# Performance work log

Hardware: AMD Instinct MI355X
Metric: run time of the kernel (lower is better)

## Reference

```python
import jax, jax.numpy as jnp
import numpy as np

EMBED = 512
HEADS = 8
HEAD_DIM = EMBED // HEADS
SCALE_BASE = 512
NEG = -1e9


def xpos_apply(x, offset, downscale):
    # x: [(b h), L, d]
    L, d = x.shape[1], x.shape[2]
    min_pos = -(L + offset) // 2
    max_pos = L + offset + min_pos
    base = (jnp.arange(0, d, 2, dtype=jnp.float32) + 0.4 * d) / (1.4 * d)      # [d/2]
    power = jnp.arange(min_pos, max_pos, dtype=jnp.float32) / SCALE_BASE        # [L']
    scale = base[None, :] ** power[:, None]                                     # [L', d/2]
    half = d // 2
    inv_freq = 1.0 / (10000.0 ** (jnp.arange(half, dtype=jnp.float32) / half))
    sinusoid = jnp.arange(scale.shape[0], dtype=jnp.float32)[:, None] * inv_freq[None, :]
    sin, cos = jnp.sin(sinusoid), jnp.cos(sinusoid)
    # keep last L rows (no-op when offset == 0)
    scale, sin, cos = scale[-L:], sin[-L:], cos[-L:]
    if downscale:
        scale = 1.0 / scale
    sin2 = jnp.repeat(sin * scale, 2, axis=-1)   # duplicate_interleave -> [L, d]
    cos2 = jnp.repeat(cos * scale, 2, axis=-1)
    x1, x2 = x[..., ::2], x[..., 1::2]
    rot = jnp.stack([-x2, x1], axis=-1).reshape(x.shape)  # rotate_every_two
    return x * cos2[None] + rot * sin2[None]


def split_heads(x, b, L):
    # 'b l (h d) -> (b h) l d'
    return x.reshape(b, L, HEADS, HEAD_DIM).transpose(0, 2, 1, 3).reshape(b * HEADS, L, HEAD_DIM)


def setup_inputs() -> dict:
    key = jax.random.key(0)
    ks = jax.random.split(key, 12)
    b, L = 4, 2048
    inp = {
        'query': jax.random.normal(ks[0], (b, L, EMBED), jnp.float32),
        'key': jax.random.normal(ks[1], (b, L, EMBED), jnp.float32),
        'value': jax.random.normal(ks[2], (b, L, EMBED), jnp.float32),
        'key_padding_mask': jnp.zeros((b, L), jnp.bool_),
        'attn_mask': jnp.where(jnp.tril(jnp.ones((L, L), jnp.bool_)), 0.0, NEG).astype(jnp.float32),
    }
    s = 1.0 / np.sqrt(EMBED)
    inp['Wq'] = jax.random.normal(ks[3], (EMBED, EMBED), jnp.float32) * s
    inp['bq'] = jnp.zeros((EMBED,), jnp.float32)
    inp['Wk'] = jax.random.normal(ks[4], (EMBED, EMBED), jnp.float32) * s
    inp['bk'] = jnp.zeros((EMBED,), jnp.float32)
    inp['Wv'] = jax.random.normal(ks[5], (EMBED, EMBED), jnp.float32) * s
    inp['bv'] = jnp.zeros((EMBED,), jnp.float32)
    inp['Wo'] = jax.random.normal(ks[6], (EMBED, EMBED), jnp.float32) * s
    inp['bo'] = jnp.zeros((EMBED,), jnp.float32)
    return inp


def reference(query, key, value, key_padding_mask, attn_mask, Wq, bq, Wk, bk, Wv, bv, Wo, bo):
    b, L, _ = query.shape
    q = split_heads(query @ Wq.T + bq, b, L)
    k = split_heads(key @ Wk.T + bk, b, L)
    v = split_heads(value @ Wv.T + bv, b, L)
    k = xpos_apply(k, 0, True)
    q = xpos_apply(q, 0, False)
    q = q * (HEAD_DIM ** -0.5)
    aw = jnp.einsum('btd,bsd->bts', q, k)                 # [(b h), t, s]
    aw = jnp.nan_to_num(aw) + attn_mask[None]
    aw = aw.reshape(b, HEADS, L, L)
    aw = jnp.where(key_padding_mask[:, None, None, :], jnp.finfo(aw.dtype).min, aw)
    aw = aw.reshape(b * HEADS, L, L)
    probs = jax.nn.softmax(aw.astype(jnp.float32), axis=-1).astype(aw.dtype)
    attn = jnp.einsum('bts,bsd->btd', probs, v)           # [(b h), t, d]
    attn = attn.reshape(b, HEADS, L, HEAD_DIM).transpose(0, 2, 1, 3).reshape(b, L, EMBED)
    return attn @ Wo.T + bo
```

## Files before the change

### kernel.cpp

```cpp
#include <hip/hip_runtime.h>
#include <hip/hip_bf16.h>

typedef __bf16 bf16x2 __attribute__((ext_vector_type(2)));
typedef __bf16 bf16x4 __attribute__((ext_vector_type(4)));
typedef __bf16 bf16x8 __attribute__((ext_vector_type(8)));
typedef float  f32x4  __attribute__((ext_vector_type(4)));

#define SEQ    2048
#define EMB    512
#define NHEAD  8
#define HD     64
#define NBATCH 4
#define MROWS  (NBATCH*SEQ)
#define QSCALE 0.18033688011112042f
#define INV2PI 0.15915494309189535f
#define TWOPI  6.28318530717958648f
#define NEGFREQ (-0.41524101186092028f)

__device__ __forceinline__ f32x4 mfma16(bf16x8 a, bf16x8 b, f32x4 c) {
  return __builtin_amdgcn_mfma_f32_16x16x32_bf16(a, b, c, 0, 0, 0);
}

typedef __attribute__((address_space(1))) const void gv_t;
typedef __attribute__((address_space(3))) void lv_t;
__device__ __forceinline__ void async16(const void* g, void* l) {
  __builtin_amdgcn_global_load_lds((gv_t*)g, (lv_t*)l, 16, 0, 0);
}

__global__ __launch_bounds__(256) void conv_kernel(const float* __restrict__ q,
                                                   const float* __restrict__ k,
                                                   const float* __restrict__ v,
                                                   const float* __restrict__ wq,
                                                   const float* __restrict__ wk,
                                                   const float* __restrict__ wv,
                                                   const float* __restrict__ wo,
                                                   __bf16* __restrict__ Qf,
                                                   __bf16* __restrict__ Kf,
                                                   __bf16* __restrict__ Vf,
                                                   __bf16* __restrict__ Wb) {
  const int z = blockIdx.y;
  const float* src;
  __bf16* dst;
  size_t i8;
  if (z < 3) {
    src = (z == 0) ? q : (z == 1) ? k : v;
    dst = (z == 0) ? Qf : (z == 1) ? Kf : Vf;
    i8 = ((size_t)blockIdx.x * 256 + threadIdx.x) * 8;
  } else {
    if (blockIdx.x >= 512) return;
    const int zw = blockIdx.x >> 7;
    src = (zw == 0) ? wq : (zw == 1) ? wk : (zw == 2) ? wv : wo;
    dst = Wb + (size_t)zw * (EMB * EMB);
    i8 = ((size_t)(blockIdx.x & 127) * 256 + threadIdx.x) * 8;
  }
  const float4 fa = ((const float4*)(src + i8))[0];
  const float4 fb = ((const float4*)(src + i8))[1];
  bf16x8 h = { (__bf16)fa.x, (__bf16)fa.y, (__bf16)fa.z, (__bf16)fa.w,
               (__bf16)fb.x, (__bf16)fb.y, (__bf16)fb.z, (__bf16)fb.w };
  *(bf16x8*)(dst + i8) = h;
}

__device__ __forceinline__ void gemm_main(const __bf16* __restrict__ A,
                                          const __bf16* __restrict__ W,
                                          __bf16* As, __bf16* Bs,
                                          f32x4 (&acc)[4][4], int m0, int n0) {
  const int tid = threadIdx.x;
  const int wid = tid >> 6, lane = tid & 63;
  const int quad = lane >> 4, l16 = lane & 15;
  const int l7 = l16 & 7;
  const int srow = lane >> 3;
  const int sxor = ((lane & 7) ^ srow) * 8;
  const int wm = (wid >> 1) * 64, wn = (wid & 1) * 64;

  #pragma unroll
  for (int i = 0; i < 4; ++i)
    #pragma unroll
    for (int j = 0; j < 4; ++j) acc[i][j] = (f32x4)(0.0f);

  for (int k0 = 0; k0 < 512; k0 += 64) {
    __syncthreads();
    #pragma unroll
    for (int ii = 0; ii < 4; ++ii) {
      const int r8 = wid * 32 + ii * 8;
      async16(A + (size_t)(m0 + r8 + srow) * 512 + k0 + sxor, &As[r8 * 64]);
      async16(W + (size_t)(n0 + r8 + srow) * 512 + k0 + sxor, &Bs[r8 * 64]);
    }
    __syncthreads();
    #pragma unroll
    for (int ks = 0; ks < 2; ++ks) {
      bf16x8 af[4], bfr[4];
      #pragma unroll
      for (int i = 0; i < 4; ++i)
        af[i] = *(const bf16x8*)&As[(wm + i * 16 + l16) * 64 +
                                    (((quad + ks * 4) ^ l7) * 8)];
      #pragma unroll
      for (int j = 0; j < 4; ++j)
        bfr[j] = *(const bf16x8*)&Bs[(wn + j * 16 + l16) * 64 +
                                     (((quad + ks * 4) ^ l7) * 8)];
      #pragma unroll
      for (int i = 0; i < 4; ++i)
        #pragma unroll
        for (int j = 0; j < 4; ++j)
          acc[i][j] = mfma16(af[i], bfr[j], acc[i][j]);
    }
  }
}

__global__ __launch_bounds__(256) void gemm_proj_kernel(
    const __bf16* __restrict__ Qf, const __bf16* __restrict__ Kf, const __bf16* __restrict__ Vf,
    const __bf16* __restrict__ Wb,
    const float* __restrict__ bq, const float* __restrict__ bk, const float* __restrict__ bv,
    __bf16* __restrict__ Qx, __bf16* __restrict__ Kx, __bf16* __restrict__ Vt) {
  __shared__ __align__(16) char smem[34816];
  __bf16* As = (__bf16*)smem;
  __bf16* Bs = (__bf16*)(smem + 16384);
  __bf16* T  = (__bf16*)smem;

  const int z = blockIdx.z;
  const __bf16* A = (z == 0) ? Qf : (z == 1) ? Kf : Vf;
  const __bf16* W = Wb + (size_t)z * (EMB * EMB);
  const float* bias = (z == 0) ? bq : (z == 1) ? bk : bv;
  const int m0 = blockIdx.y * 128, n0 = blockIdx.x * 128;

  f32x4 acc[4][4];
  gemm_main(A, W, As, Bs, acc, m0, n0);

  const int tid = threadIdx.x;
  const int wid = tid >> 6, lane = tid & 63;
  const int quad = lane >> 4, l16 = lane & 15;
  const int wm = (wid >> 1) * 64, wn = (wid & 1) * 64;

  __syncthreads();

  if (z == 2) {
    #pragma unroll
    for (int j = 0; j < 4; ++j) {
      const float bval = bias[n0 + wn + j * 16 + l16];
      #pragma unroll
      for (int i = 0; i < 4; ++i) {
        bf16x4 p = { (__bf16)(acc[i][j][0] + bval), (__bf16)(acc[i][j][1] + bval),
                     (__bf16)(acc[i][j][2] + bval), (__bf16)(acc[i][j][3] + bval) };
        *(bf16x4*)&T[(wn + j * 16 + l16) * 136 + wm + i * 16 + quad * 4] = p;
      }
    }
    __syncthreads();
    const int nrow = tid >> 1, mh = (tid & 1) << 6;
    bf16x8 vv[8];
    #pragma unroll
    for (int u = 0; u < 8; ++u) vv[u] = *(const bf16x8*)&T[nrow * 136 + mh + u * 8];
    const int n = n0 + nrow, h = n >> 6, d = n & 63;
    const int bb = m0 >> 11, lb2 = (m0 & 2047) + mh;
    __bf16* dst = Vt + ((size_t)(bb * 8 + h) * 64 + d) * 2048 + lb2;
    #pragma unroll
    for (int u = 0; u < 8; ++u) *(bf16x8*)(dst + u * 8) = vv[u];
  } else {
    #pragma unroll
    for (int j = 0; j < 4; ++j) {
      const float bval = bias[n0 + wn + j * 16 + l16];
      #pragma unroll
      for (int i = 0; i < 4; ++i)
        #pragma unroll
        for (int r = 0; r < 4; ++r)
          T[(wm + i * 16 + quad * 4 + r) * 136 + wn + j * 16 + l16] =
              (__bf16)(acc[i][j][r] + bval);
    }
    __syncthreads();
    const int lrow = tid >> 1, half = tid & 1;
    const int gm = m0 + lrow, l = gm & 2047, bb = gm >> 11;
    const int h = (n0 >> 6) + half;
    bf16x8 vv[8];
    #pragma unroll
    for (int u = 0; u < 8; ++u)
      vv[u] = *(const bf16x8*)&T[lrow * 136 + half * 64 + u * 8];
    bf16x8 ov[8];
    const float lf = (float)l;
    const float pw = (lf - 1024.0f) * (1.0f / 512.0f);
    const float qs = (z == 0) ? QSCALE : 1.0f;
    #pragma unroll
    for (int i = 0; i < 32; ++i) {
      const float x1 = (float)vv[i >> 2][(2 * i) & 7];
      const float x2 = (float)vv[i >> 2][(2 * i + 1) & 7];
      const float lb = __log2f((2.0f * i + 25.6f) * (1.0f / 89.6f));
      const float e  = (z == 0) ? (pw * lb) : (-pw * lb);
      const float sc = __builtin_amdgcn_exp2f(e) * qs;
      const float ang = lf * __builtin_amdgcn_exp2f((float)i * NEGFREQ);
      float rev = ang * INV2PI;
      rev -= floorf(rev);
      const float ar = rev * TWOPI;
      const float sn = __sinf(ar) * sc;
      const float cs = __cosf(ar) * sc;
      ov[i >> 2][(2 * i) & 7]     = (__bf16)(x1 * cs - x2 * sn);
      ov[i >> 2][(2 * i + 1) & 7] = (__bf16)(x2 * cs + x1 * sn);
    }
    __bf16* dst = ((z == 0) ? Qx : Kx) + ((size_t)(bb * 8 + h) * 2048 + l) * 64;
    #pragma unroll
    for (int u = 0; u < 8; ++u) *(bf16x8*)(dst + u * 8) = ov[u];
  }
}

__global__ __launch_bounds__(256) void gemm_out_kernel(
    const __bf16* __restrict__ A, const __bf16* __restrict__ W,
    const float* __restrict__ bias, float* __restrict__ C) {
  __shared__ __align__(16) char smem[34816];
  __bf16* As = (__bf16*)smem;
  __bf16* Bs = (__bf16*)(smem + 16384);
  const int m0 = blockIdx.y * 128, n0 = blockIdx.x * 128;
  f32x4 acc[4][4];
  gemm_main(A, W, As, Bs, acc, m0, n0);
  const int tid = threadIdx.x;
  const int wid = tid >> 6, lane = tid & 63;
  const int quad = lane >> 4, l16 = lane & 15;
  const int wm = (wid >> 1) * 64, wn = (wid & 1) * 64;
  #pragma unroll
  for (int j = 0; j < 4; ++j) {
    const int n = n0 + wn + j * 16 + l16;
    const float bval = bias[n];
    #pragma unroll
    for (int i = 0; i < 4; ++i)
      #pragma unroll
      for (int r = 0; r < 4; ++r)
        C[(size_t)(m0 + wm + i * 16 + quad * 4 + r) * 512 + n] = acc[i][j][r] + bval;
  }
}

__global__ __launch_bounds__(256) void flash_kernel(const __bf16* __restrict__ Qx,
                                                    const __bf16* __restrict__ Kx,
                                                    const __bf16* __restrict__ Vt,
                                                    const unsigned char* __restrict__ kpm,
                                                    __bf16* __restrict__ Oa,
                                                    float* __restrict__ PartO,
                                                    float* __restrict__ Pml) {
  __shared__ __align__(16) __bf16 Ks[2][64 * HD];
  __shared__ __align__(16) __bf16 Vs[2][64 * HD];
  __shared__ __align__(16) __bf16 Qs[64 * HD];

  const int tid = threadIdx.x;
  const int wid = tid >> 6;
  const int lane = tid & 63;
  const int quad = lane >> 4;
  const int l16 = lane & 15;
  const int l7 = l16 & 7;
  const int srow = lane >> 3;
  const int sxor = ((lane & 7) ^ srow) * 8;
  const int bh = blockIdx.x;
  const int b = bh >> 3;
  const int y = blockIdx.y;

  int qb, it0, it1, split;
  if (y < 32) {
    qb = 31 - (y >> 1);
    split = 1;
    const int nt = qb + 1, hh = nt >> 1;
    if ((y & 1) == 0) { it0 = 0;  it1 = hh; }
    else              { it0 = hh; it1 = nt; }
  } else {
    qb = 47 - y;
    split = 0;
    it0 = 0; it1 = qb + 1;
  }
  const int q0 = qb * 64;

  const __bf16* Qbase = Qx + (size_t)bh * (SEQ * HD);
  const __bf16* Kbase = Kx + (size_t)bh * (SEQ * HD);
  const __bf16* Vbase = Vt + (size_t)bh * (HD * SEQ);
  __bf16* Pw = Qs + wid * 1024;

  #pragma unroll
  for (int ii = 0; ii < 2; ++ii) {
    const int r0 = wid * 16 + ii * 8;
    async16(Qbase + (size_t)(q0 + r0 + srow) * HD + sxor, &Qs[r0 * HD]);
    async16(Kbase + (size_t)(it0 * 64 + r0 + srow) * HD + sxor, &Ks[0][r0 * HD]);
    async16(Vbase + (size_t)(r0 + srow) * SEQ + it0 * 64 + sxor, &Vs[0][r0 * HD]);
  }
  __syncthreads();
  const bf16x8 qf0 = *(const bf16x8*)&Qs[(wid * 16 + l16) * HD + ((quad ^ l7) * 8)];
  const bf16x8 qf1 = *(const bf16x8*)&Qs[(wid * 16 + l16) * HD + (((quad + 4) ^ l7) * 8)];

  f32x4 o[4];
  #pragma unroll
  for (int i = 0; i < 4; ++i) o[i] = (f32x4)(0.0f);
  float m_run = -1e30f, l_run = 0.0f;
  const int myq = q0 + wid * 16 + l16;

  for (int it = it0; it < it1; ++it) {
    const int kv0 = it << 6;
    const int cur = (it - it0) & 1;
    const __bf16* Kc = &Ks[cur][0];
    const __bf16* Vc = &Vs[cur][0];

    if (it + 1 < it1) {
      const int kn = kv0 + 64;
      #pragma unroll
      for (int ii = 0; ii < 2; ++ii) {
        const int r0 = wid * 16 + ii * 8;
        async16(Kbase + (size_t)(kn + r0 + srow) * HD + sxor, &Ks[cur ^ 1][r0 * HD]);
        async16(Vbase + (size_t)(r0 + srow) * SEQ + kn + sxor, &Vs[cur ^ 1][r0 * HD]);
      }
    }
    const unsigned mine =
        *(const unsigned*)(kpm + b * SEQ + kv0 + ((lane & 15) << 2));

    f32x4 s[4];
    #pragma unroll
    for (int nb = 0; nb < 4; ++nb) s[nb] = (f32x4)(0.0f);
    __builtin_amdgcn_s_setprio(1);
    #pragma unroll
    for (int nb = 0; nb < 4; ++nb) {
      const bf16x8 kf = *(const bf16x8*)&Kc[(nb * 16 + l16) * HD + ((quad ^ l7) * 8)];
      s[nb] = mfma16(kf, qf0, s[nb]);
    }
    #pragma unroll
    for (int nb = 0; nb < 4; ++nb) {
      const bf16x8 kf = *(const bf16x8*)&Kc[(nb * 16 + l16) * HD + (((quad + 4) ^ l7) * 8)];
      s[nb] = mfma16(kf, qf1, s[nb]);
    }
    __builtin_amdgcn_s_setprio(0);

    if (kv0 + 63 > q0 + wid * 16) {
      #pragma unroll
      for (int nb = 0; nb < 4; ++nb)
        #pragma unroll
        for (int r = 0; r < 4; ++r)
          if (kv0 + nb * 16 + quad * 4 + r > myq) s[nb][r] = -1e30f;
    }
    if (__any(mine != 0)) {
      const unsigned char* kp0 = kpm + b * SEQ + kv0;
      #pragma unroll
      for (int nb = 0; nb < 4; ++nb) {
        const unsigned pk = *(const unsigned*)(kp0 + nb * 16 + quad * 4);
        if (pk) {
          if (pk & 0x000000FFu) s[nb][0] = -1e30f;
          if (pk & 0x0000FF00u) s[nb][1] = -1e30f;
          if (pk & 0x00FF0000u) s[nb][2] = -1e30f;
          if (pk & 0xFF000000u) s[nb][3] = -1e30f;
        }
      }
    }

    float mx;
    {
      f32x4 u0, u1;
      #pragma unroll
      for (int r = 0; r < 4; ++r) u0[r] = fmaxf(s[0][r], s[1][r]);
      #pragma unroll
      for (int r = 0; r < 4; ++r) u1[r] = fmaxf(s[2][r], s[3][r]);
      #pragma unroll
      for (int r = 0; r < 4; ++r) u0[r] = fmaxf(u0[r], u1[r]);
      mx = fmaxf(fmaxf(u0[0], u0[1]), fmaxf(u0[2], u0[3]));
    }
    if (__any(mx > m_run)) {
      float rm = fmaxf(mx, __shfl_xor(mx, 16));
      rm = fmaxf(rm, __shfl_xor(rm, 32));
      const float m_new = fmaxf(m_run, rm);
      const float alpha = __builtin_amdgcn_exp2f(m_run - m_new);
      #pragma unroll
      for (int i = 0; i < 4; ++i) o[i] *= alpha;
      l_run *= alpha;
      m_run = m_new;
    }
    #pragma unroll
    for (int nb = 0; nb < 4; ++nb)
      #pragma unroll
      for (int r = 0; r < 4; ++r)
        s[nb][r] = __builtin_amdgcn_exp2f(s[nb][r] - m_run);
    {
      f32x4 v01 = s[0] + s[1];
      f32x4 v23 = s[2] + s[3];
      f32x4 vt = v01 + v23;
      l_run += (vt[0] + vt[1]) + (vt[2] + vt[3]);
    }

    #pragma unroll
    for (int nb = 0; nb < 4; ++nb) {
      bf16x4 p4 = { (__bf16)s[nb][0], (__bf16)s[nb][1],
                    (__bf16)s[nb][2], (__bf16)s[nb][3] };
      *(bf16x4*)&Pw[l16 * 64 + (((nb * 2 + (quad >> 1)) ^ l7) << 3) + (quad & 1) * 4] = p4;
    }

    __builtin_amdgcn_s_setprio(1);
    #pragma unroll
    for (int ks = 0; ks < 2; ++ks) {
      const bf16x8 pf = *(const bf16x8*)&Pw[l16 * 64 + (((ks * 4 + quad) ^ l7) << 3)];
      const int bx = ((quad + ks * 4) ^ l7) * 8;
      #pragma unroll
      for (int j = 0; j < 4; ++j)
        o[j] = mfma16(*(const bf16x8*)&Vc[(j * 16 + l16) * HD + bx], pf, o[j]);
    }
    __builtin_amdgcn_s_setprio(0);

    if (it + 1 < it1) __syncthreads();
  }

  float lt = l_run + __shfl_xor(l_run, 16);
  lt += __shfl_xor(lt, 32);

  if (split) {
    const int tile = (bh * 16 + (qb - 16)) * 2 + (y & 1);
    float* po = PartO + (size_t)tile * 4096;
    #pragma unroll
    for (int i = 0; i < 4; ++i)
      #pragma unroll
      for (int r = 0; r < 4; ++r)
        po[(i * 16 + quad * 4 + r) * 64 + wid * 16 + l16] = o[i][r];
    if (quad == 0) {
      Pml[(size_t)tile * 128 + wid * 16 + l16] = m_run;
      Pml[(size_t)tile * 128 + 64 + wid * 16 + l16] = lt;
    }
    return;
  }

  const float inv_l = 1.0f / lt;
  {
    bf16x4 t0 = { (__bf16)(o[0][0] * inv_l), (__bf16)(o[0][1] * inv_l),
                  (__bf16)(o[0][2] * inv_l), (__bf16)(o[0][3] * inv_l) };
    bf16x4 t1 = { (__bf16)(o[1][0] * inv_l), (__bf16)(o[1][1] * inv_l),
                  (__bf16)(o[1][2] * inv_l), (__bf16)(o[1][3] * inv_l) };
    bf16x4 t2 = { (__bf16)(o[2][0] * inv_l), (__bf16)(o[2][1] * inv_l),
                  (__bf16)(o[2][2] * inv_l), (__bf16)(o[2][3] * inv_l) };
    bf16x4 t3 = { (__bf16)(o[3][0] * inv_l), (__bf16)(o[3][1] * inv_l),
                  (__bf16)(o[3][2] * inv_l), (__bf16)(o[3][3] * inv_l) };
    *(bf16x4*)&Pw[l16 * 64 + (((0 + (quad >> 1)) ^ l7) << 3) + (quad & 1) * 4] = t0;
    *(bf16x4*)&Pw[l16 * 64 + (((2 + (quad >> 1)) ^ l7) << 3) + (quad & 1) * 4] = t1;
    *(bf16x4*)&Pw[l16 * 64 + (((4 + (quad >> 1)) ^ l7) << 3) + (quad & 1) * 4] = t2;
    *(bf16x4*)&Pw[l16 * 64 + (((6 + (quad >> 1)) ^ l7) << 3) + (quad & 1) * 4] = t3;
  }
  const int h = bh & 7;
  #pragma unroll
  for (int ii = 0; ii < 2; ++ii) {
    const int qr = ii * 8 + (lane >> 3);
    const bf16x8 ovv = *(const bf16x8*)&Pw[qr * 64 + (((lane & 7) ^ (qr & 7)) << 3)];
    *(bf16x8*)(Oa + (((size_t)b * SEQ + q0 + wid * 16 + qr) * NHEAD + h) * HD +
               (lane & 7) * 8) = ovv;
  }
}

__global__ __launch_bounds__(256) void combine_kernel(const float* __restrict__ PartO,
                                                      const float* __restrict__ Pml,
                                                      __bf16* __restrict__ Oa) {
  __shared__ __align__(16) __bf16 T[64 * 72];
  const int pair = blockIdx.x;
  const int bh = pair >> 4, qb = 16 + (pair & 15);
  const int b = bh >> 3, h = bh & 7, q0 = qb * 64;
  const float* P0 = PartO + (size_t)pair * 2 * 4096;
  const float* P1 = P0 + 4096;
  const float* ml = Pml + (size_t)pair * 2 * 128;
  const int t = threadIdx.x;
  const int d = t >> 2, qg = (t & 3) * 16;

  float w0[16], w1[16];
  #pragma unroll
  for (int k = 0; k < 16; ++k) {
    const float m0 = ml[qg + k],       l0 = ml[64 + qg + k];
    const float m1 = ml[128 + qg + k], l1 = ml[192 + qg + k];
    const float m = fmaxf(m0, m1);
    const float a0 = __builtin_amdgcn_exp2f(m0 - m);
    const float a1 = __builtin_amdgcn_exp2f(m1 - m);
    const float inv = 1.0f / (a0 * l0 + a1 * l1);
    w0[k] = a0 * inv;
    w1[k] = a1 * inv;
  }
  #pragma unroll
  for (int k = 0; k < 16; ++k) {
    const float v = P0[d * 64 + qg + k] * w0[k] + P1[d * 64 + qg + k] * w1[k];
    T[(qg + k) * 72 + d] = (__bf16)v;
  }
  __syncthreads();
  const int q = t >> 2, dg = (t & 3) * 16;
  const bf16x8 va = *(const bf16x8*)&T[q * 72 + dg];
  const bf16x8 vb = *(const bf16x8*)&T[q * 72 + dg + 8];
  __bf16* dst = Oa + (((size_t)b * SEQ + q0 + q) * NHEAD + h) * HD + dg;
  *(bf16x8*)dst = va;
  *(bf16x8*)(dst + 8) = vb;
}

extern "C" void kernel_launch(void* const* d_in, const int* in_sizes, int n_in,
                              void* d_out, int out_size, void* d_ws, size_t ws_size,
                              hipStream_t stream) {
  (void)in_sizes; (void)n_in; (void)out_size; (void)ws_size;
  const float* query = (const float*)d_in[0];
  const float* key   = (const float*)d_in[1];
  const float* value = (const float*)d_in[2];
  const unsigned char* kpm = (const unsigned char*)d_in[3];
  const float* Wq = (const float*)d_in[5];
  const float* bq = (const float*)d_in[6];
  const float* Wk = (const float*)d_in[7];
  const float* bk = (const float*)d_in[8];
  const float* Wv = (const float*)d_in[9];
  const float* bv = (const float*)d_in[10];
  const float* Wo = (const float*)d_in[11];
  const float* bo = (const float*)d_in[12];
  float* out = (float*)d_out;

  char* ws = (char*)d_ws;
  const size_t SZ = (size_t)MROWS * EMB * 2;
  __bf16* Qf = (__bf16*)(ws);
  __bf16* Kf = (__bf16*)(ws + SZ);
  __bf16* Vf = (__bf16*)(ws + 2 * SZ);
  __bf16* Qx = (__bf16*)(ws + 3 * SZ);
  __bf16* Kx = (__bf16*)(ws + 4 * SZ);
  __bf16* Vt = (__bf16*)(ws + 5 * SZ);
  __bf16* Wb = (__bf16*)(ws + 6 * SZ);
  __bf16* Oa = Qf;
  float* PartO = (float*)(ws + SZ);
  float* Pml = out;

  conv_kernel<<<dim3(2048, 4), dim3(256), 0, stream>>>(
      query, key, value, Wq, Wk, Wv, Wo, Qf, Kf, Vf, Wb);
  gemm_proj_kernel<<<dim3(4, 64, 3), dim3(256), 0, stream>>>(
      Qf, Kf, Vf, Wb, bq, bk, bv, Qx, Kx, Vt);
  flash_kernel<<<dim3(32, 48), dim3(256), 0, stream>>>(
      Qx, Kx, Vt, kpm, Oa, PartO, Pml);
  combine_kernel<<<dim3(512), dim3(256), 0, stream>>>(PartO, Pml, Oa);
  gemm_out_kernel<<<dim3(4, 64), dim3(256), 0, stream>>>(
      Oa, Wb + (size_t)3 * EMB * EMB, bo, out);
}
```

Measured before the change: 221.9 us.

## Load K/V fragments directly from global memory and drop split-KV combine kernel

The flash kernel stops staging K and V tiles in double-buffered shared memory with async copies and block barriers. Each wave now loads its MFMA operand fragments straight from global memory into registers, which relies on L2/L1 for the reuse across the four waves. The split-KV scheme for the long query blocks and the separate combine kernel are removed, so each block walks its full causal range, and launch bounds request four blocks per CU. This removes barriers, LDS traffic and one kernel launch plus the partial-result round trip. In exchange the long-row blocks see worse load balance, and repeated global loads may be latency-bound.

```diff
diff --git a/kernel.cpp b/kernel.cpp
--- a/kernel.cpp
+++ b/kernel.cpp
@@ -223,16 +223,12 @@
   }
 }
 
-__global__ __launch_bounds__(256) void flash_kernel(const __bf16* __restrict__ Qx,
-                                                    const __bf16* __restrict__ Kx,
-                                                    const __bf16* __restrict__ Vt,
-                                                    const unsigned char* __restrict__ kpm,
-                                                    __bf16* __restrict__ Oa,
-                                                    float* __restrict__ PartO,
-                                                    float* __restrict__ Pml) {
-  __shared__ __align__(16) __bf16 Ks[2][64 * HD];
-  __shared__ __align__(16) __bf16 Vs[2][64 * HD];
-  __shared__ __align__(16) __bf16 Qs[64 * HD];
+__global__ __launch_bounds__(256, 4) void flash_kernel(const __bf16* __restrict__ Qx,
+                                                       const __bf16* __restrict__ Kx,
+                                                       const __bf16* __restrict__ Vt,
+                                                       const unsigned char* __restrict__ kpm,
+                                                       __bf16* __restrict__ Oa) {
+  __shared__ __align__(16) __bf16 Ps[4 * 1024];
 
   const int tid = threadIdx.x;
   const int wid = tid >> 6;
@@ -240,41 +236,26 @@
   const int quad = lane >> 4;
   const int l16 = lane & 15;
   const int l7 = l16 & 7;
-  const int srow = lane >> 3;
-  const int sxor = ((lane & 7) ^ srow) * 8;
   const int bh = blockIdx.x;
   const int b = bh >> 3;
-  const int y = blockIdx.y;
-
-  int qb, it0, it1, split;
-  if (y < 32) {
-    qb = 31 - (y >> 1);
-    split = 1;
-    const int nt = qb + 1, hh = nt >> 1;
-    if ((y & 1) == 0) { it0 = 0;  it1 = hh; }
-    else              { it0 = hh; it1 = nt; }
-  } else {
-    qb = 47 - y;
-    split = 0;
-    it0 = 0; it1 = qb + 1;
-  }
+  const int qb = 31 - (int)blockIdx.y;
   const int q0 = qb * 64;
-
-  const __bf16* Qbase = Qx + (size_t)bh * (SEQ * HD);
-  const __bf16* Kbase = Kx + (size_t)bh * (SEQ * HD);
-  const __bf16* Vbase = Vt + (size_t)bh * (HD * SEQ);
-  __bf16* Pw = Qs + wid * 1024;
-
-  #pragma unroll
-  for (int ii = 0; ii < 2; ++ii) {
-    const int r0 = wid * 16 + ii * 8;
-    async16(Qbase + (size_t)(q0 + r0 + srow) * HD + sxor, &Qs[r0 * HD]);
-    async16(Kbase + (size_t)(it0 * 64 + r0 + srow) * HD + sxor, &Ks[0][r0 * HD]);
-    async16(Vbase + (size_t)(r0 + srow) * SEQ + it0 * 64 + sxor, &Vs[0][r0 * HD]);
-  }
-  __syncthreads();
-  const bf16x8 qf0 = *(const bf16x8*)&Qs[(wid * 16 + l16) * HD + ((quad ^ l7) * 8)];
-  const bf16x8 qf1 = *(const bf16x8*)&Qs[(wid * 16 + l16) * HD + (((quad + 4) ^ l7) * 8)];
+  __bf16* Pw = Ps + wid * 1024;
+
+  const __bf16* Qrow = Qx + (size_t)bh * (SEQ * HD) +
+                       (size_t)(q0 + wid * 16 + l16) * HD + quad * 8;
+  const bf16x8 qf0 = *(const bf16x8*)(Qrow);
+  const bf16x8 qf1 = *(const bf16x8*)(Qrow + 32);
+
+  const __bf16* Kb = Kx + (size_t)bh * (SEQ * HD);
+  const __bf16* Vb = Vt + (size_t)bh * (HD * SEQ);
+  int koff  = l16 * HD + quad * 8;
+  int koff2 = koff + 2048;
+  int voff0 = l16 * SEQ + quad * 8;
+  int voff1 = voff0 + 16 * SEQ;
+  int voff2 = voff0 + 32 * SEQ;
+  int voff3 = voff0 + 48 * SEQ;
+  const unsigned char* kpb = kpm + b * SEQ + (l16 << 2);
 
   f32x4 o[4];
   #pragma unroll
@@ -282,38 +263,41 @@
   float m_run = -1e30f, l_run = 0.0f;
   const int myq = q0 + wid * 16 + l16;
 
-  for (int it = it0; it < it1; ++it) {
+  for (int it = 0; it <= qb; ++it) {
     const int kv0 = it << 6;
-    const int cur = (it - it0) & 1;
-    const __bf16* Kc = &Ks[cur][0];
-    const __bf16* Vc = &Vs[cur][0];
-
-    if (it + 1 < it1) {
-      const int kn = kv0 + 64;
-      #pragma unroll
-      for (int ii = 0; ii < 2; ++ii) {
-        const int r0 = wid * 16 + ii * 8;
-        async16(Kbase + (size_t)(kn + r0 + srow) * HD + sxor, &Ks[cur ^ 1][r0 * HD]);
-        async16(Vbase + (size_t)(r0 + srow) * SEQ + kn + sxor, &Vs[cur ^ 1][r0 * HD]);
-      }
-    }
-    const unsigned mine =
-        *(const unsigned*)(kpm + b * SEQ + kv0 + ((lane & 15) << 2));
+
+    const bf16x8 kf00 = *(const bf16x8*)(Kb + koff);
+    const bf16x8 kf01 = *(const bf16x8*)(Kb + koff + 32);
+    const bf16x8 kf10 = *(const bf16x8*)(Kb + koff + 1024);
+    const bf16x8 kf11 = *(const bf16x8*)(Kb + koff + 1056);
+    const bf16x8 kf20 = *(const bf16x8*)(Kb + koff2);
+    const bf16x8 kf21 = *(const bf16x8*)(Kb + koff2 + 32);
+    const bf16x8 kf30 = *(const bf16x8*)(Kb + koff2 + 1024);
+    const bf16x8 kf31 = *(const bf16x8*)(Kb + koff2 + 1056);
+
+    const bf16x8 vf00 = *(const bf16x8*)(Vb + voff0);
+    const bf16x8 vf01 = *(const bf16x8*)(Vb + voff0 + 32);
+    const bf16x8 vf10 = *(const bf16x8*)(Vb + voff1);
+    const bf16x8 vf11 = *(const bf16x8*)(Vb + voff1 + 32);
+    const bf16x8 vf20 = *(const bf16x8*)(Vb + voff2);
+    const bf16x8 vf21 = *(const bf16x8*)(Vb + voff2 + 32);
+    const bf16x8 vf30 = *(const bf16x8*)(Vb + voff3);
+    const bf16x8 vf31 = *(const bf16x8*)(Vb + voff3 + 32);
+
+    const unsigned mine = *(const unsigned*)(kpb + kv0);
 
     f32x4 s[4];
     #pragma unroll
     for (int nb = 0; nb < 4; ++nb) s[nb] = (f32x4)(0.0f);
     __builtin_amdgcn_s_setprio(1);
-    #pragma unroll
-    for (int nb = 0; nb < 4; ++nb) {
-      const bf16x8 kf = *(const bf16x8*)&Kc[(nb * 16 + l16) * HD + ((quad ^ l7) * 8)];
-      s[nb] = mfma16(kf, qf0, s[nb]);
-    }
-    #pragma unroll
-    for (int nb = 0; nb < 4; ++nb) {
-      const bf16x8 kf = *(const bf16x8*)&Kc[(nb * 16 + l16) * HD + (((quad + 4) ^ l7) * 8)];
-      s[nb] = mfma16(kf, qf1, s[nb]);
-    }
+    s[0] = mfma16(kf00, qf0, s[0]);
+    s[1] = mfma16(kf10, qf0, s[1]);
+    s[2] = mfma16(kf20, qf0, s[2]);
+    s[3] = mfma16(kf30, qf0, s[3]);
+    s[0] = mfma16(kf01, qf1, s[0]);
+    s[1] = mfma16(kf11, qf1, s[1]);
+    s[2] = mfma16(kf21, qf1, s[2]);
+    s[3] = mfma16(kf31, qf1, s[3]);
     __builtin_amdgcn_s_setprio(0);
 
     if (kv0 + 63 > q0 + wid * 16) {
@@ -377,37 +361,27 @@
       *(bf16x4*)&Pw[l16 * 64 + (((nb * 2 + (quad >> 1)) ^ l7) << 3) + (quad & 1) * 4] = p4;
     }
 
+    const bf16x8 pf0 = *(const bf16x8*)&Pw[l16 * 64 + ((quad ^ l7) << 3)];
     __builtin_amdgcn_s_setprio(1);
-    #pragma unroll
-    for (int ks = 0; ks < 2; ++ks) {
-      const bf16x8 pf = *(const bf16x8*)&Pw[l16 * 64 + (((ks * 4 + quad) ^ l7) << 3)];
-      const int bx = ((quad + ks * 4) ^ l7) * 8;
-      #pragma unroll
-      for (int j = 0; j < 4; ++j)
-        o[j] = mfma16(*(const bf16x8*)&Vc[(j * 16 + l16) * HD + bx], pf, o[j]);
-    }
+    o[0] = mfma16(vf00, pf0, o[0]);
+    o[1] = mfma16(vf10, pf0, o[1]);
+    o[2] = mfma16(vf20, pf0, o[2]);
+    o[3] = mfma16(vf30, pf0, o[3]);
     __builtin_amdgcn_s_setprio(0);
-
-    if (it + 1 < it1) __syncthreads();
+    const bf16x8 pf1 = *(const bf16x8*)&Pw[l16 * 64 + (((4 + quad) ^ l7) << 3)];
+    __builtin_amdgcn_s_setprio(1);
+    o[0] = mfma16(vf01, pf1, o[0]);
+    o[1] = mfma16(vf11, pf1, o[1]);
+    o[2] = mfma16(vf21, pf1, o[2]);
+    o[3] = mfma16(vf31, pf1, o[3]);
+    __builtin_amdgcn_s_setprio(0);
+
+    koff  += 64 * HD; koff2 += 64 * HD;
+    voff0 += 64; voff1 += 64; voff2 += 64; voff3 += 64;
   }
 
   float lt = l_run + __shfl_xor(l_run, 16);
   lt += __shfl_xor(lt, 32);
-
-  if (split) {
-    const int tile = (bh * 16 + (qb - 16)) * 2 + (y & 1);
-    float* po = PartO + (size_t)tile * 4096;
-    #pragma unroll
-    for (int i = 0; i < 4; ++i)
-      #pragma unroll
-      for (int r = 0; r < 4; ++r)
-        po[(i * 16 + quad * 4 + r) * 64 + wid * 16 + l16] = o[i][r];
-    if (quad == 0) {
-      Pml[(size_t)tile * 128 + wid * 16 + l16] = m_run;
-      Pml[(size_t)tile * 128 + 64 + wid * 16 + l16] = lt;
-    }
-    return;
-  }
 
   const float inv_l = 1.0f / lt;
   {
@@ -432,45 +406,6 @@
     *(bf16x8*)(Oa + (((size_t)b * SEQ + q0 + wid * 16 + qr) * NHEAD + h) * HD +
                (lane & 7) * 8) = ovv;
   }
-}
-
-__global__ __launch_bounds__(256) void combine_kernel(const float* __restrict__ PartO,
-                                                      const float* __restrict__ Pml,
-                                                      __bf16* __restrict__ Oa) {
-  __shared__ __align__(16) __bf16 T[64 * 72];
-  const int pair = blockIdx.x;
-  const int bh = pair >> 4, qb = 16 + (pair & 15);
-  const int b = bh >> 3, h = bh & 7, q0 = qb * 64;
-  const float* P0 = PartO + (size_t)pair * 2 * 4096;
-  const float* P1 = P0 + 4096;
-  const float* ml = Pml + (size_t)pair * 2 * 128;
-  const int t = threadIdx.x;
-  const int d = t >> 2, qg = (t & 3) * 16;
-
-  float w0[16], w1[16];
-  #pragma unroll
-  for (int k = 0; k < 16; ++k) {
-    const float m0 = ml[qg + k],       l0 = ml[64 + qg + k];
-    const float m1 = ml[128 + qg + k], l1 = ml[192 + qg + k];
-    const float m = fmaxf(m0, m1);
-    const float a0 = __builtin_amdgcn_exp2f(m0 - m);
-    const float a1 = __builtin_amdgcn_exp2f(m1 - m);
-    const float inv = 1.0f / (a0 * l0 + a1 * l1);
-    w0[k] = a0 * inv;
-    w1[k] = a1 * inv;
-  }
-  #pragma unroll
-  for (int k = 0; k < 16; ++k) {
-    const float v = P0[d * 64 + qg + k] * w0[k] + P1[d * 64 + qg + k] * w1[k];
-    T[(qg + k) * 72 + d] = (__bf16)v;
-  }
-  __syncthreads();
-  const int q = t >> 2, dg = (t & 3) * 16;
-  const bf16x8 va = *(const bf16x8*)&T[q * 72 + dg];
-  const bf16x8 vb = *(const bf16x8*)&T[q * 72 + dg + 8];
-  __bf16* dst = Oa + (((size_t)b * SEQ + q0 + q) * NHEAD + h) * HD + dg;
-  *(bf16x8*)dst = va;
-  *(bf16x8*)(dst + 8) = vb;
 }
 
 extern "C" void kernel_launch(void* const* d_in, const int* in_sizes, int n_in,
@@ -501,16 +436,12 @@
   __bf16* Vt = (__bf16*)(ws + 5 * SZ);
   __bf16* Wb = (__bf16*)(ws + 6 * SZ);
   __bf16* Oa = Qf;
-  float* PartO = (float*)(ws + SZ);
-  float* Pml = out;
 
   conv_kernel<<<dim3(2048, 4), dim3(256), 0, stream>>>(
       query, key, value, Wq, Wk, Wv, Wo, Qf, Kf, Vf, Wb);
   gemm_proj_kernel<<<dim3(4, 64, 3), dim3(256), 0, stream>>>(
       Qf, Kf, Vf, Wb, bq, bk, bv, Qx, Kx, Vt);
-  flash_kernel<<<dim3(32, 48), dim3(256), 0, stream>>>(
-      Qx, Kx, Vt, kpm, Oa, PartO, Pml);
-  combine_kernel<<<dim3(512), dim3(256), 0, stream>>>(PartO, Pml, Oa);
+  flash_kernel<<<dim3(32, 32), dim3(256), 0, stream>>>(Qx, Kx, Vt, kpm, Oa);
   gemm_out_kernel<<<dim3(4, 64), dim3(256), 0, stream>>>(
       Oa, Wb + (size_t)3 * EMB * EMB, bo, out);
 }
```

After: 310.6 us. 1.4x slower.
